# Kernel tuning notes

Measured on AMD Instinct MI355X. Metric: run time of the kernel, lower is better.

The kernel has to match this reference:

```python
import jax, jax.numpy as jnp
import numpy as np
from jax import lax

EPS = 1e-6
DT_RANK = 24  # ceil(384/16), Mamba convention
D_STATE = 16


def _ln(x, g, b, eps=EPS):
    m = jnp.mean(x, axis=-1, keepdims=True)
    v = jnp.mean((x - m) ** 2, axis=-1, keepdims=True)
    return (x - m) * lax.rsqrt(v + eps) * g + b


def setup_inputs() -> dict:
    key = jax.random.key(0)
    ks = jax.random.split(key, 10)
    B, Dd, Hh, Ww, C = 2, 8, 16, 16, 384
    di, ds, r = 384, D_STATE, DT_RANK  # d_inner = expand * d_model = 384
    s = 0.02
    f = lambda k, shape: (jax.random.normal(k, shape, jnp.float32) * s)
    return {
        "x": jax.random.normal(ks[0], (B, Dd, Hh, Ww, C), jnp.float32),
        "g1": jnp.ones((C,), jnp.float32), "b1": jnp.zeros((C,), jnp.float32),
        "W_in": f(ks[1], (C, 2 * di)), "b_in": jnp.zeros((2 * di,), jnp.float32),
        "conv_w": f(ks[2], (di, 1, 3, 3, 3)), "conv_b": jnp.zeros((di,), jnp.float32),
        "W_x": f(ks[3], (di, r + 2 * ds)),
        "W_dt": f(ks[4], (r, di)), "b_dt": jnp.zeros((di,), jnp.float32),
        "A_log": jnp.tile(jnp.log(jnp.arange(1, ds + 1, dtype=jnp.float32)), (di, 1)),
        "D_skip": jnp.ones((di,), jnp.float32),
        "on_g": jnp.ones((di,), jnp.float32), "on_b": jnp.zeros((di,), jnp.float32),
        "W_out": f(ks[5], (di, C)), "b_out": jnp.zeros((C,), jnp.float32),
        "g2": jnp.ones((C,), jnp.float32), "b2": jnp.zeros((C,), jnp.float32),
        "W1": f(ks[6], (C, C)), "b1m": jnp.zeros((C,), jnp.float32),
        "W2": f(ks[7], (C, C)), "b2m": jnp.zeros((C,), jnp.float32),
    }


def _ss3d(h, W_in, b_in, conv_w, conv_b, W_x, W_dt, b_dt, A_log, D_skip, on_g, on_b, W_out, b_out):
    # h: [B, D, H, W, C] -> Mamba-style selective scan over flattened DHW (orientation 0)
    B, Dd, Hh, Ww, C = h.shape
    di = W_in.shape[1] // 2
    ds = D_STATE
    L = Dd * Hh * Ww
    seq = h.reshape(B, L, C)
    xz = seq @ W_in + b_in                      # [B, L, 2*di]
    xin, z = jnp.split(xz, 2, axis=-1)
    # depthwise 3D conv + SiLU on the x branch
    xc = xin.reshape(B, Dd, Hh, Ww, di).transpose(0, 4, 1, 2, 3)  # [B, di, D, H, W]
    xc = lax.conv_general_dilated(xc, conv_w, (1, 1, 1), 'SAME',
                                  feature_group_count=di,
                                  dimension_numbers=('NCDHW', 'OIDHW', 'NCDHW'))
    xc = xc + conv_b[None, :, None, None, None]
    xin = jax.nn.silu(xc).transpose(0, 2, 3, 4, 1).reshape(B, L, di)
    # input-dependent dt, B, C
    dbc = xin @ W_x                              # [B, L, r + 2*ds]
    dt, Bm, Cm = jnp.split(dbc, [DT_RANK, DT_RANK + ds], axis=-1)
    dt = jax.nn.softplus(dt @ W_dt + b_dt)       # [B, L, di]
    A = -jnp.exp(A_log)                          # [di, ds]
    dA = jnp.exp(dt[..., None] * A)              # [B, L, di, ds]
    dBx = dt[..., None] * Bm[:, :, None, :] * xin[..., None]  # [B, L, di, ds]

    def step(carry, inp):
        da, dbx, c = inp                         # [B,di,ds], [B,di,ds], [B,ds]
        carry = da * carry + dbx
        y = jnp.einsum('bds,bs->bd', carry, c)
        return carry, y

    xs = (dA.transpose(1, 0, 2, 3), dBx.transpose(1, 0, 2, 3), Cm.transpose(1, 0, 2))
    h0 = jnp.zeros((B, di, ds), dA.dtype)
    _, ys = lax.scan(step, h0, xs)               # ys: [L, B, di]
    y = ys.transpose(1, 0, 2) + xin * D_skip
    y = _ln(y, on_g, on_b) * jax.nn.silu(z)
    out = y @ W_out + b_out
    return out.reshape(B, Dd, Hh, Ww, C)


def reference(x, g1, b1, W_in, b_in, conv_w, conv_b, W_x, W_dt, b_dt, A_log, D_skip,
              on_g, on_b, W_out, b_out, g2, b2, W1, b1m, W2, b2m):
    # x + SS3D(LN(x)); then x + MLP(LN(x)).  drop_path/dropout = 0 (eval)
    a = _ss3d(_ln(x, g1, b1), W_in, b_in, conv_w, conv_b, W_x, W_dt, b_dt,
              A_log, D_skip, on_g, on_b, W_out, b_out)
    x1 = x + a
    h2 = _ln(x1, g2, b2)
    mlp = jax.nn.gelu(h2 @ W1 + b1m) @ W2 + b2m
    return x1 + mlp
```

## Files before the change

kernel.cpp:

```cpp
#include <hip/hip_runtime.h>
#include <hip/hip_bf16.h>

using bf16 = __hip_bfloat16;
#define DEV __device__ __forceinline__

typedef __attribute__((ext_vector_type(8))) short short8;
typedef __attribute__((ext_vector_type(8))) unsigned short ushort8;
typedef __attribute__((ext_vector_type(4))) float f32x4;

constexpr int Bb = 2, DD = 8, HH = 16, WW = 16;
constexpr int C = 384, DI = 384, DS = 16, RR = 24;
constexpr int L = DD * HH * WW;
constexpr int M = Bb * L;

DEV bf16 f2b(float v) { return __float2bfloat16(v); }
DEV unsigned short f2bu(float v) {
    bf16 t = __float2bfloat16(v);
    unsigned short u; __builtin_memcpy(&u, &t, 2); return u;
}
DEV float braw(unsigned short u) {
    unsigned int x = ((unsigned int)u) << 16;
    float f; __builtin_memcpy(&f, &x, 4); return f;
}
DEV bool isbf(const unsigned short* g1p) { return g1p[0] == 0x3F80; }

typedef const __attribute__((address_space(1))) unsigned int* gaddr_t;
typedef __attribute__((address_space(3))) unsigned int* laddr_t;
DEV void gload_lds16(const void* g, void* l) {
    __builtin_amdgcn_global_load_lds((gaddr_t)g, (laddr_t)l, 16, 0, 0);
}

DEV float wred64(float v) {
    #pragma unroll
    for (int off = 32; off > 0; off >>= 1) v += __shfl_xor(v, off, 64);
    return v;
}
DEV float siluf(float x) { return x / (1.0f + __expf(-x)); }
DEV float softplusf(float x) { return (x > 15.0f) ? x : log1pf(__expf(x)); }
DEV float gelu_tanh(float x) {
    const float k0 = 0.7978845608028654f;
    float u = k0 * (x + 0.044715f * x * x * x);
    float e = __expf(2.0f * u);
    float t = 1.0f - 2.0f / (e + 1.0f);
    return 0.5f * x * (1.0f + t);
}

struct PrepTab {
    const void* tsrc[4];
    unsigned short* tdst[4];
    int tK[4], tN[4];
    const void* csrc[17];
    float* cdst[17];
    int coff[18];
};
__global__ __launch_bounds__(256) void prep_k(PrepTab t,
                                              const unsigned short* __restrict__ g1p,
                                              int ctotal) {
    bool fl = isbf(g1p);
    int z = blockIdx.z;
    if (z < 4) {
        __shared__ unsigned short tt[32][33];
        int N = t.tN[z], K = t.tK[z];
        int n0 = blockIdx.x * 32, k0 = blockIdx.y * 32;
        if (n0 >= N || k0 >= K) return;
        const void* src = t.tsrc[z];
        unsigned short* dst = t.tdst[z];
        int tx = threadIdx.x & 31, ty = threadIdx.x >> 5;
        #pragma unroll
        for (int i = 0; i < 4; i++) {
            int k = k0 + ty + i * 8;
            unsigned short u;
            if (fl) u = ((const unsigned short*)src)[(size_t)k * N + n0 + tx];
            else    u = f2bu(((const float*)src)[(size_t)k * N + n0 + tx]);
            tt[ty + i * 8][tx] = u;
        }
        __syncthreads();
        #pragma unroll
        for (int i = 0; i < 4; i++) {
            int n = n0 + ty + i * 8;
            dst[(size_t)n * K + k0 + tx] = tt[tx][ty + i * 8];
        }
    } else {
        int i = (blockIdx.y * 24 + blockIdx.x) * 256 + threadIdx.x;
        if (i >= ctotal) return;
        int seg = 0;
        #pragma unroll
        for (int k = 1; k < 18; k++) seg += (i >= t.coff[k]) ? 1 : 0;
        int j = i - t.coff[seg];
        const void* s = t.csrc[seg];
        float v = fl ? braw(((const unsigned short*)s)[j]) : ((const float*)s)[j];
        t.cdst[seg][j] = v;
    }
}

template <bool RAWIN>
__global__ __launch_bounds__(256) void ln_k(const void* __restrict__ xr,
                                            const float* __restrict__ g,
                                            const float* __restrict__ b,
                                            bf16* __restrict__ out,
                                            const unsigned short* __restrict__ g1p) {
    bool fl = RAWIN ? isbf(g1p) : false;
    int wave = blockIdx.x * 4 + (threadIdx.x >> 6);
    int lane = threadIdx.x & 63;
    size_t base = (size_t)wave * C;
    float v[6];
    #pragma unroll
    for (int j = 0; j < 6; j++) {
        size_t idx = base + lane + 64 * j;
        if (RAWIN && fl) v[j] = braw(((const unsigned short*)xr)[idx]);
        else             v[j] = ((const float*)xr)[idx];
    }
    float s = 0.f;
    #pragma unroll
    for (int j = 0; j < 6; j++) s += v[j];
    s = wred64(s);
    float mean = s * (1.0f / C);
    float q = 0.f;
    #pragma unroll
    for (int j = 0; j < 6; j++) { float d = v[j] - mean; q += d * d; }
    q = wred64(q);
    float rstd = rsqrtf(q * (1.0f / C) + 1e-6f);
    #pragma unroll
    for (int j = 0; j < 6; j++) {
        int c = lane + 64 * j;
        out[base + c] = f2b((v[j] - mean) * rstd * g[c] + b[c]);
    }
}

enum { EPI_XZT = 0, EPI_OUT = 1, EPI_GELU = 2, EPI_FINAL = 3 };

template <int N, int TN, int EPI>
__global__ __launch_bounds__(256) void gemm_mfma(const bf16* __restrict__ A,
                                                 const unsigned short* __restrict__ Bt,
                                                 const float* __restrict__ bias,
                                                 float* __restrict__ o0,
                                                 float* __restrict__ o1,
                                                 const float* __restrict__ auxf,
                                                 const void* __restrict__ auxraw,
                                                 void* __restrict__ obf,
                                                 const unsigned short* __restrict__ g1p) {
    __shared__ unsigned short Asb[128 * 32];
    __shared__ unsigned short Bsb[TN * 32];
    constexpr int MT = (TN == 128) ? 4 : 2;
    int tid = threadIdx.x;
    int m0 = blockIdx.x * 128, n0 = blockIdx.y * TN;
    int wid = tid >> 6, lane = tid & 63;
    int wm = (TN == 128) ? (wid >> 1) * 64 : wid * 32;
    int wn = (TN == 128) ? (wid & 1) * 64 : 0;
    int quad = lane >> 4, l15 = lane & 15;
    f32x4 acc[MT][4] = {};
    int srow = tid >> 2, sseg = (tid & 3) * 8;
    const unsigned short* Au = (const unsigned short*)A;
    for (int k0 = 0; k0 < 384; k0 += 32) {
        __syncthreads();
        gload_lds16(Au + (size_t)(m0 + srow) * 384 + k0 + sseg,
                    &Asb[srow * 32 + sseg]);
        gload_lds16(Au + (size_t)(m0 + 64 + srow) * 384 + k0 + sseg,
                    &Asb[(64 + srow) * 32 + sseg]);
        gload_lds16(Bt + (size_t)(n0 + srow) * 384 + k0 + sseg,
                    &Bsb[srow * 32 + sseg]);
        if constexpr (TN == 128)
            gload_lds16(Bt + (size_t)(n0 + 64 + srow) * 384 + k0 + sseg,
                        &Bsb[(64 + srow) * 32 + sseg]);
        __syncthreads();
        short8 af[MT], bfr[4];
        #pragma unroll
        for (int mt = 0; mt < MT; mt++)
            af[mt] = *(const short8*)&Asb[(wm + mt * 16 + l15) * 32 + quad * 8];
        #pragma unroll
        for (int nt = 0; nt < 4; nt++)
            bfr[nt] = *(const short8*)&Bsb[(wn + nt * 16 + l15) * 32 + quad * 8];
        #pragma unroll
        for (int mt = 0; mt < MT; mt++)
            #pragma unroll
            for (int nt = 0; nt < 4; nt++)
                acc[mt][nt] = __builtin_amdgcn_mfma_f32_16x16x32_bf16(
                    af[mt], bfr[nt], acc[mt][nt], 0, 0, 0);
    }
    bool fl = (EPI == EPI_FINAL || EPI == EPI_OUT) ? isbf(g1p) : false;
    #pragma unroll
    for (int mt = 0; mt < MT; mt++) {
        #pragma unroll
        for (int nt = 0; nt < 4; nt++) {
            int n = n0 + wn + nt * 16 + l15;
            int mb = m0 + wm + mt * 16 + quad * 4;
            float bi = bias[n];
            if constexpr (EPI == EPI_XZT) {
                f32x4 v = acc[mt][nt];
                v[0] += bi; v[1] += bi; v[2] += bi; v[3] += bi;
                float* dst = (n < 384) ? (o0 + (size_t)n * M + mb)
                                       : (o1 + (size_t)(n - 384) * M + mb);
                *(f32x4*)dst = v;
            } else {
                #pragma unroll
                for (int r = 0; r < 4; r++) {
                    int m = mb + r;
                    float v = acc[mt][nt][r] + bi;
                    if constexpr (EPI == EPI_OUT) {
                        float av;
                        if (fl) av = braw(((const unsigned short*)auxraw)[(size_t)m * 384 + n]);
                        else    av = ((const float*)auxraw)[(size_t)m * 384 + n];
                        o0[(size_t)m * 384 + n] = v + av;
                    } else if constexpr (EPI == EPI_GELU) {
                        ((bf16*)obf)[(size_t)m * 384 + n] = f2b(gelu_tanh(v));
                    } else {
                        float rr = v + auxf[(size_t)m * 384 + n];
                        if (fl) ((bf16*)obf)[(size_t)m * 384 + n] = f2b(rr);
                        else    ((float*)obf)[(size_t)m * 384 + n] = rr;
                    }
                }
            }
        }
    }
}

__global__ __launch_bounds__(256) void convT_k(const float* __restrict__ xT,
                                               const float* __restrict__ cw,
                                               const float* __restrict__ cb,
                                               float* __restrict__ xinT) {
    int c = blockIdx.y;
    int m0 = (blockIdx.x * 256 + threadIdx.x) * 4;
    int l = m0 & (L - 1);
    int d = l >> 8, h = (l >> 4) & 15, w0 = l & 15;
    const float* xc = xT + (size_t)c * M;
    const float* wc = cw + c * 27;
    float bias = cb[c];
    float acc[4] = {bias, bias, bias, bias};
    #pragma unroll
    for (int kd = -1; kd <= 1; kd++) {
        int dd = d + kd; if ((unsigned)dd >= 8u) continue;
        #pragma unroll
        for (int kh = -1; kh <= 1; kh++) {
            int hh = h + kh; if ((unsigned)hh >= 16u) continue;
            int mm = m0 + kd * 256 + kh * 16;
            float vv[6];
            vv[0] = (w0 == 0) ? 0.f : xc[mm - 1];
            float4 v14 = *(const float4*)(xc + mm);
            vv[1] = v14.x; vv[2] = v14.y; vv[3] = v14.z; vv[4] = v14.w;
            vv[5] = (w0 == 12) ? 0.f : xc[mm + 4];
            const float* wk = wc + (kd + 1) * 9 + (kh + 1) * 3;
            float wa = wk[0], wb = wk[1], wcc = wk[2];
            #pragma unroll
            for (int j = 0; j < 4; j++)
                acc[j] = fmaf(vv[j], wa, fmaf(vv[j + 1], wb, fmaf(vv[j + 2], wcc, acc[j])));
        }
    }
    float4 o = make_float4(siluf(acc[0]), siluf(acc[1]), siluf(acc[2]), siluf(acc[3]));
    *(float4*)(xinT + (size_t)c * M + m0) = o;
}

__global__ __launch_bounds__(256) void dbc2_k(const float* __restrict__ xinT,
                                              const float* __restrict__ Wx,
                                              float* __restrict__ part) {
    __shared__ float As[16][64];
    __shared__ float Ws[16 * 56];
    int tid = threadIdx.x;
    int m0 = blockIdx.x * 64;
    int kc = blockIdx.y;
    int tm = tid & 63, grp = tid >> 6;
    int kk = tid >> 4, mc = (tid & 15) * 4;
    float acc[14] = {};
    for (int k0 = kc * 64; k0 < kc * 64 + 64; k0 += 16) {
        float4 av = *(const float4*)(xinT + (size_t)(k0 + kk) * M + m0 + mc);
        __syncthreads();
        *(float4*)&As[kk][mc] = av;
        for (int idx = tid; idx < 16 * 56; idx += 256)
            Ws[idx] = Wx[k0 * 56 + idx];
        __syncthreads();
        #pragma unroll
        for (int k = 0; k < 16; k++) {
            float a = As[k][tm];
            #pragma unroll
            for (int jj = 0; jj < 14; jj++)
                acc[jj] = fmaf(a, Ws[k * 56 + grp * 14 + jj], acc[jj]);
        }
    }
    int m = m0 + tm;
    #pragma unroll
    for (int jj = 0; jj < 14; jj++) {
        int col = grp * 14 + jj;
        part[((size_t)kc * 56 + col) * M + m] = acc[jj];
    }
}

__global__ __launch_bounds__(256) void dbcfin_k(const float* __restrict__ part,
                                                const float* __restrict__ Wdt,
                                                const float* __restrict__ bdt,
                                                float* __restrict__ dtT,
                                                unsigned short* __restrict__ Brow,
                                                unsigned short* __restrict__ Crow) {
    __shared__ float dtr[24][64];
    int tid = threadIdx.x;
    int m0 = blockIdx.x * 64;
    int ng = blockIdx.y;
    for (int i = tid; i < 24 * 64; i += 256) {
        int col = i >> 6, mm = i & 63;
        float s = 0.f;
        #pragma unroll
        for (int kc = 0; kc < 6; kc++)
            s += part[((size_t)kc * 56 + col) * M + m0 + mm];
        dtr[col][mm] = s;
    }
    if (ng == 0) {
        for (int i = tid; i < 32 * 64; i += 256) {
            int col = 24 + (i >> 6), mm = i & 63;
            float s = 0.f;
            #pragma unroll
            for (int kc = 0; kc < 6; kc++)
                s += part[((size_t)kc * 56 + col) * M + m0 + mm];
            int m = m0 + mm;
            if (col < 40) Brow[(size_t)m * 16 + col - 24] = f2bu(s);
            else          Crow[(size_t)m * 16 + col - 40] = f2bu(s);
        }
    }
    __syncthreads();
    int mm = tid & 63, nq = tid >> 6;
    #pragma unroll 4
    for (int nj = 0; nj < 16; nj++) {
        int n = ng * 64 + nq * 16 + nj;
        float acc = bdt[n];
        #pragma unroll
        for (int j = 0; j < 24; j++)
            acc = fmaf(dtr[j][mm], Wdt[j * 384 + n], acc);
        dtT[(size_t)n * M + m0 + mm] = softplusf(acc);
    }
}

__global__ __launch_bounds__(128) void scan4_k(const float* __restrict__ dtT,
                                               const float* __restrict__ xinT,
                                               const unsigned short* __restrict__ Brow,
                                               const unsigned short* __restrict__ Crow,
                                               const float* __restrict__ alog,
                                               const float* __restrict__ dsk,
                                               float* __restrict__ yT) {
    __shared__ float dt_s[2112], x_s[2112];
    __shared__ float ypart[2 * 2112];
    int bi = blockIdx.x;
    int b = bi / DI, d = bi % DI;
    int wave = threadIdx.x >> 6, lane = threadIdx.x & 63;
    int s0 = wave * 8;
    float Aneg[8];
    #pragma unroll
    for (int ss = 0; ss < 8; ss++) Aneg[ss] = -__expf(alog[d * DS + s0 + ss]);
    const float* dtp = dtT + (size_t)d * M + b * L;
    const float* xp  = xinT + (size_t)d * M + b * L;
    #pragma unroll
    for (int i = 0; i < 4; i++) {
        int t4 = (threadIdx.x + i * 128) * 4;
        float4 dv = *(const float4*)(dtp + t4);
        float4 xv = *(const float4*)(xp + t4);
        int base = t4 + (t4 >> 5);
        dt_s[base + 0] = dv.x; dt_s[base + 1] = dv.y;
        dt_s[base + 2] = dv.z; dt_s[base + 3] = dv.w;
        x_s[base + 0] = xv.x; x_s[base + 1] = xv.y;
        x_s[base + 2] = xv.z; x_s[base + 3] = xv.w;
    }
    __syncthreads();
    const unsigned short* Bp = Brow + ((size_t)b * L) * 16 + s0;
    const unsigned short* Cp = Crow + ((size_t)b * L) * 16 + s0;
    int tbase = lane * 32;
    int pbase = lane * 33;
    float Ap[8], Bg[8];
    #pragma unroll
    for (int ss = 0; ss < 8; ss++) { Ap[ss] = 1.f; Bg[ss] = 0.f; }
    #pragma unroll 4
    for (int j = 0; j < 32; j++) {
        float dtv = dt_s[pbase + j];
        float dxv = dtv * x_s[pbase + j];
        ushort8 bu = *(const ushort8*)(Bp + (size_t)(tbase + j) * 16);
        #pragma unroll
        for (int ss = 0; ss < 8; ss++) {
            float dA = __expf(dtv * Aneg[ss]);
            Bg[ss] = fmaf(dA, Bg[ss], dxv * braw(bu[ss]));
            Ap[ss] *= dA;
        }
    }
    float carry[8];
    #pragma unroll
    for (int ss = 0; ss < 8; ss++) {
        float a = Ap[ss], bb = Bg[ss];
        #pragma unroll
        for (int off = 1; off < 64; off <<= 1) {
            float ap = __shfl_up(a, off, 64);
            float bp = __shfl_up(bb, off, 64);
            if (lane >= off) { bb = fmaf(a, bp, bb); a *= ap; }
        }
        float c = __shfl_up(bb, 1, 64);
        carry[ss] = (lane == 0) ? 0.f : c;
    }
    float* ypw = ypart + wave * 2112;
    float h[8];
    #pragma unroll
    for (int ss = 0; ss < 8; ss++) h[ss] = carry[ss];
    #pragma unroll 4
    for (int j = 0; j < 32; j++) {
        float dtv = dt_s[pbase + j];
        float dxv = dtv * x_s[pbase + j];
        size_t toff = (size_t)(tbase + j) * 16;
        ushort8 bu = *(const ushort8*)(Bp + toff);
        ushort8 cu = *(const ushort8*)(Cp + toff);
        float acc = 0.f;
        #pragma unroll
        for (int ss = 0; ss < 8; ss++) {
            float dA = __expf(dtv * Aneg[ss]);
            h[ss] = fmaf(dA, h[ss], dxv * braw(bu[ss]));
            acc = fmaf(h[ss], braw(cu[ss]), acc);
        }
        ypw[pbase + j] = acc;
    }
    __syncthreads();
    float Dv = dsk[d];
    float* yp = yT + (size_t)d * M + b * L;
    #pragma unroll
    for (int i = 0; i < 16; i++) {
        int t = threadIdx.x + 128 * i;
        int ti = t + (t >> 5);
        yp[t] = fmaf(x_s[ti], Dv, ypart[ti] + ypart[2112 + ti]);
    }
}

__global__ __launch_bounds__(256) void lnmulT_k(const float* __restrict__ yT,
                                                const float* __restrict__ zT,
                                                const float* __restrict__ g,
                                                const float* __restrict__ b,
                                                unsigned short* __restrict__ yact) {
    __shared__ float rs1[8][32], rs2[8][32];
    __shared__ float meanb[32], rstdb[32];
    __shared__ unsigned short tile[32][392];
    int moff = threadIdx.x & 31;
    int dsub = threadIdx.x >> 5;
    int m0 = blockIdx.x * 32;
    size_t mg = m0 + moff;
    float s1 = 0.f, s2 = 0.f;
    #pragma unroll 8
    for (int j = 0; j < 48; j++) {
        int d = dsub + 8 * j;
        float v = yT[(size_t)d * M + mg];
        s1 += v; s2 += v * v;
    }
    rs1[dsub][moff] = s1;
    rs2[dsub][moff] = s2;
    __syncthreads();
    if (threadIdx.x < 32) {
        float a1 = 0.f, a2 = 0.f;
        #pragma unroll
        for (int ss = 0; ss < 8; ss++) { a1 += rs1[ss][threadIdx.x]; a2 += rs2[ss][threadIdx.x]; }
        float mean = a1 * (1.0f / DI);
        float var = a2 * (1.0f / DI) - mean * mean;
        meanb[threadIdx.x] = mean;
        rstdb[threadIdx.x] = rsqrtf(var + 1e-6f);
    }
    __syncthreads();
    float mean = meanb[moff], rstd = rstdb[moff];
    #pragma unroll 8
    for (int j = 0; j < 48; j++) {
        int d = dsub + 8 * j;
        float v = yT[(size_t)d * M + mg];
        float ln = (v - mean) * rstd * g[d] + b[d];
        float zv = zT[(size_t)d * M + mg];
        tile[moff][d] = f2bu(ln * siluf(zv));
    }
    __syncthreads();
    #pragma unroll
    for (int i = 0; i < 6; i++) {
        int chunk = threadIdx.x + 256 * i;
        int row = chunk / 48, cc = chunk % 48;
        *(uint4*)(yact + ((size_t)(m0 + row)) * 384 + cc * 8) =
            *(const uint4*)&tile[row][cc * 8];
    }
}

extern "C" void kernel_launch(void* const* d_in, const int* in_sizes, int n_in,
                              void* d_out, int out_size, void* d_ws, size_t ws_size,
                              hipStream_t stream) {
    float* ws = (float*)d_ws;
    constexpr size_t S = (size_t)M * 384;
    bf16*  hb   = (bf16*)ws;
    float* xT   = ws + S / 2;
    float* zT   = xT + S;
    float* xinT = zT + S;
    float* dtT  = xinT + S;
    float* x1   = dtT + S;
    unsigned short* Brow = (unsigned short*)(x1 + S);
    unsigned short* Crow = Brow + (size_t)M * 16;
    float* part = (float*)(Crow + (size_t)M * 16);
    float* smalls = part + (size_t)6 * 56 * M;

    float* g1f  = smalls;        float* b1f  = g1f + 384;
    float* binf = b1f + 384;     float* cwf  = binf + 768;
    float* cbf  = cwf + 10368;   float* wxf  = cbf + 384;
    float* wdtf = wxf + 21504;   float* bdtf = wdtf + 9216;
    float* alogf= bdtf + 384;    float* dskf = alogf + 6144;
    float* ongf = dskf + 384;    float* onbf = ongf + 384;
    float* boutf= onbf + 384;    float* g2f  = boutf + 384;
    float* b2f_ = g2f + 384;     float* b1mf = b2f_ + 384;
    float* b2mf = b1mf + 384;
    unsigned short* WinT  = (unsigned short*)(b2mf + 384);
    unsigned short* WoutT = WinT + 294912;
    unsigned short* W1T   = WoutT + 147456;
    unsigned short* W2T   = W1T + 147456;

    float* yT = xT;
    bf16* h2b = hb;
    unsigned short* yactb = (unsigned short*)dtT;
    unsigned short* m1b = (unsigned short*)zT;
    const unsigned short* g1p = (const unsigned short*)d_in[1];

    PrepTab tab;
    {
        tab.tsrc[0] = d_in[3];  tab.tdst[0] = WinT;  tab.tK[0] = 384; tab.tN[0] = 768;
        tab.tsrc[1] = d_in[14]; tab.tdst[1] = WoutT; tab.tK[1] = 384; tab.tN[1] = 384;
        tab.tsrc[2] = d_in[18]; tab.tdst[2] = W1T;   tab.tK[2] = 384; tab.tN[2] = 384;
        tab.tsrc[3] = d_in[20]; tab.tdst[3] = W2T;   tab.tK[3] = 384; tab.tN[3] = 384;
        int idxs[17] = {1, 2, 4, 5, 6, 7, 8, 9, 10, 11, 12, 13, 15, 16, 17, 19, 21};
        float* dsts[17] = {g1f, b1f, binf, cwf, cbf, wxf, wdtf, bdtf, alogf, dskf,
                           ongf, onbf, boutf, g2f, b2f_, b1mf, b2mf};
        int ns[17] = {384, 384, 768, 10368, 384, 21504, 9216, 384, 6144, 384,
                      384, 384, 384, 384, 384, 384, 384};
        int off = 0;
        for (int k = 0; k < 17; k++) {
            tab.csrc[k] = d_in[idxs[k]];
            tab.cdst[k] = dsts[k];
            tab.coff[k] = off;
            off += ns[k];
        }
        tab.coff[17] = off;
        prep_k<<<dim3(24, 12, 5), 256, 0, stream>>>(tab, g1p, off);
    }

    ln_k<true><<<M / 4, 256, 0, stream>>>(d_in[0], g1f, b1f, hb, g1p);
    gemm_mfma<768, 128, EPI_XZT><<<dim3(M / 128, 6), 256, 0, stream>>>(
        hb, WinT, binf, xT, zT, nullptr, nullptr, nullptr, g1p);
    convT_k<<<dim3(M / 1024, DI), 256, 0, stream>>>(xT, cwf, cbf, xinT);
    dbc2_k<<<dim3(M / 64, 6), 256, 0, stream>>>(xinT, wxf, part);
    dbcfin_k<<<dim3(M / 64, 6), 256, 0, stream>>>(part, wdtf, bdtf, dtT, Brow, Crow);
    scan4_k<<<Bb * DI, 128, 0, stream>>>(dtT, xinT, Brow, Crow, alogf, dskf, yT);
    lnmulT_k<<<M / 32, 256, 0, stream>>>(yT, zT, ongf, onbf, yactb);
    gemm_mfma<384, 64, EPI_OUT><<<dim3(M / 128, 6), 256, 0, stream>>>(
        (const bf16*)yactb, WoutT, boutf, x1, nullptr, nullptr, d_in[0], nullptr, g1p);
    ln_k<false><<<M / 4, 256, 0, stream>>>(x1, g2f, b2f_, h2b, g1p);
    gemm_mfma<384, 64, EPI_GELU><<<dim3(M / 128, 6), 256, 0, stream>>>(
        h2b, W1T, b1mf, nullptr, nullptr, nullptr, nullptr, m1b, g1p);
    gemm_mfma<384, 64, EPI_FINAL><<<dim3(M / 128, 6), 256, 0, stream>>>(
        (const bf16*)m1b, W2T, b2mf, nullptr, nullptr, x1, nullptr, d_out, g1p);
}
```

Before: 232.0 us.

## Fuse first LayerNorm into prep kernel and second LayerNorm into out-projection GEMM

The first LayerNorm now runs as extra blocks (z==5) of the weight-prep kernel. It reads g1/b1 straight from the raw inputs, so it no longer waits on the converted copies and saves one launch. The output-projection GEMM is replaced by a full-row kernel: each block owns 64 rows and all 384 columns. It adds the residual, writes x1, and computes the second LayerNorm in registers with shuffle reductions, removing the separate ln_k pass and the re-read of x1. In exchange the fused GEMM has only 64 blocks, with large accumulator register use and a big B tile in LDS per block. It also computes variance as E[x²]−mean², which is less numerically stable.

```diff
diff --git a/kernel.cpp b/kernel.cpp
--- a/kernel.cpp
+++ b/kernel.cpp
@@ -54,14 +54,19 @@
     int coff[18];
 };
 __global__ __launch_bounds__(256) void prep_k(PrepTab t,
+                                              const void* __restrict__ xraw,
+                                              const void* __restrict__ g1raw,
+                                              const void* __restrict__ b1raw,
+                                              bf16* __restrict__ hb,
                                               const unsigned short* __restrict__ g1p,
                                               int ctotal) {
     bool fl = isbf(g1p);
     int z = blockIdx.z;
     if (z < 4) {
+        if (blockIdx.x >= 288) return;
         __shared__ unsigned short tt[32][33];
         int N = t.tN[z], K = t.tK[z];
-        int n0 = blockIdx.x * 32, k0 = blockIdx.y * 32;
+        int n0 = (blockIdx.x % 24) * 32, k0 = (blockIdx.x / 24) * 32;
         if (n0 >= N || k0 >= K) return;
         const void* src = t.tsrc[z];
         unsigned short* dst = t.tdst[z];
@@ -80,8 +85,8 @@
             int n = n0 + ty + i * 8;
             dst[(size_t)n * K + k0 + tx] = tt[tx][ty + i * 8];
         }
-    } else {
-        int i = (blockIdx.y * 24 + blockIdx.x) * 256 + threadIdx.x;
+    } else if (z == 4) {
+        int i = blockIdx.x * 256 + threadIdx.x;
         if (i >= ctotal) return;
         int seg = 0;
         #pragma unroll
@@ -90,44 +95,41 @@
         const void* s = t.csrc[seg];
         float v = fl ? braw(((const unsigned short*)s)[j]) : ((const float*)s)[j];
         t.cdst[seg][j] = v;
-    }
-}
-
-template <bool RAWIN>
-__global__ __launch_bounds__(256) void ln_k(const void* __restrict__ xr,
-                                            const float* __restrict__ g,
-                                            const float* __restrict__ b,
-                                            bf16* __restrict__ out,
-                                            const unsigned short* __restrict__ g1p) {
-    bool fl = RAWIN ? isbf(g1p) : false;
-    int wave = blockIdx.x * 4 + (threadIdx.x >> 6);
-    int lane = threadIdx.x & 63;
-    size_t base = (size_t)wave * C;
-    float v[6];
-    #pragma unroll
-    for (int j = 0; j < 6; j++) {
-        size_t idx = base + lane + 64 * j;
-        if (RAWIN && fl) v[j] = braw(((const unsigned short*)xr)[idx]);
-        else             v[j] = ((const float*)xr)[idx];
-    }
-    float s = 0.f;
-    #pragma unroll
-    for (int j = 0; j < 6; j++) s += v[j];
-    s = wred64(s);
-    float mean = s * (1.0f / C);
-    float q = 0.f;
-    #pragma unroll
-    for (int j = 0; j < 6; j++) { float d = v[j] - mean; q += d * d; }
-    q = wred64(q);
-    float rstd = rsqrtf(q * (1.0f / C) + 1e-6f);
-    #pragma unroll
-    for (int j = 0; j < 6; j++) {
-        int c = lane + 64 * j;
-        out[base + c] = f2b((v[j] - mean) * rstd * g[c] + b[c]);
-    }
-}
-
-enum { EPI_XZT = 0, EPI_OUT = 1, EPI_GELU = 2, EPI_FINAL = 3 };
+    } else {
+        int wave = blockIdx.x * 4 + (threadIdx.x >> 6);
+        int lane = threadIdx.x & 63;
+        size_t base = (size_t)wave * C;
+        float v[6];
+        #pragma unroll
+        for (int j = 0; j < 6; j++) {
+            size_t idx = base + lane + 64 * j;
+            if (fl) v[j] = braw(((const unsigned short*)xraw)[idx]);
+            else    v[j] = ((const float*)xraw)[idx];
+        }
+        float s = 0.f;
+        #pragma unroll
+        for (int j = 0; j < 6; j++) s += v[j];
+        s = wred64(s);
+        float mean = s * (1.0f / C);
+        float q = 0.f;
+        #pragma unroll
+        for (int j = 0; j < 6; j++) { float d = v[j] - mean; q += d * d; }
+        q = wred64(q);
+        float rstd = rsqrtf(q * (1.0f / C) + 1e-6f);
+        #pragma unroll
+        for (int j = 0; j < 6; j++) {
+            int c = lane + 64 * j;
+            float gv, bv;
+            if (fl) { gv = braw(((const unsigned short*)g1raw)[c]);
+                      bv = braw(((const unsigned short*)b1raw)[c]); }
+            else    { gv = ((const float*)g1raw)[c];
+                      bv = ((const float*)b1raw)[c]; }
+            hb[base + c] = f2b((v[j] - mean) * rstd * gv + bv);
+        }
+    }
+}
+
+enum { EPI_XZT = 0, EPI_GELU = 2, EPI_FINAL = 3 };
 
 template <int N, int TN, int EPI>
 __global__ __launch_bounds__(256) void gemm_mfma(const bf16* __restrict__ A,
@@ -136,7 +138,6 @@
                                                  float* __restrict__ o0,
                                                  float* __restrict__ o1,
                                                  const float* __restrict__ auxf,
-                                                 const void* __restrict__ auxraw,
                                                  void* __restrict__ obf,
                                                  const unsigned short* __restrict__ g1p) {
     __shared__ unsigned short Asb[128 * 32];
@@ -177,7 +178,7 @@
                 acc[mt][nt] = __builtin_amdgcn_mfma_f32_16x16x32_bf16(
                     af[mt], bfr[nt], acc[mt][nt], 0, 0, 0);
     }
-    bool fl = (EPI == EPI_FINAL || EPI == EPI_OUT) ? isbf(g1p) : false;
+    bool fl = (EPI == EPI_FINAL) ? isbf(g1p) : false;
     #pragma unroll
     for (int mt = 0; mt < MT; mt++) {
         #pragma unroll
@@ -196,12 +197,7 @@
                 for (int r = 0; r < 4; r++) {
                     int m = mb + r;
                     float v = acc[mt][nt][r] + bi;
-                    if constexpr (EPI == EPI_OUT) {
-                        float av;
-                        if (fl) av = braw(((const unsigned short*)auxraw)[(size_t)m * 384 + n]);
-                        else    av = ((const float*)auxraw)[(size_t)m * 384 + n];
-                        o0[(size_t)m * 384 + n] = v + av;
-                    } else if constexpr (EPI == EPI_GELU) {
+                    if constexpr (EPI == EPI_GELU) {
                         ((bf16*)obf)[(size_t)m * 384 + n] = f2b(gelu_tanh(v));
                     } else {
                         float rr = v + auxf[(size_t)m * 384 + n];
@@ -210,6 +206,85 @@
                     }
                 }
             }
+        }
+    }
+}
+
+__global__ __launch_bounds__(256) void gemmout_ln_k(
+        const unsigned short* __restrict__ A,
+        const unsigned short* __restrict__ Bt,
+        const float* __restrict__ bias,
+        const void* __restrict__ resid,
+        const float* __restrict__ g,
+        const float* __restrict__ b,
+        float* __restrict__ x1,
+        bf16* __restrict__ h2,
+        const unsigned short* __restrict__ g1p) {
+    __shared__ unsigned short Asb[64 * 32];
+    __shared__ unsigned short Bsb[384 * 32];
+    int tid = threadIdx.x;
+    int m0 = blockIdx.x * 64;
+    int wid = tid >> 6, lane = tid & 63;
+    int quad = lane >> 4, l15 = lane & 15;
+    f32x4 acc[24] = {};
+    int srow = tid >> 2, sseg = (tid & 3) * 8;
+    for (int k0 = 0; k0 < 384; k0 += 32) {
+        __syncthreads();
+        gload_lds16(A + (size_t)(m0 + srow) * 384 + k0 + sseg, &Asb[srow * 32 + sseg]);
+        #pragma unroll
+        for (int c = 0; c < 6; c++)
+            gload_lds16(Bt + (size_t)(c * 64 + srow) * 384 + k0 + sseg,
+                        &Bsb[(c * 64 + srow) * 32 + sseg]);
+        __syncthreads();
+        short8 af = *(const short8*)&Asb[(wid * 16 + l15) * 32 + quad * 8];
+        #pragma unroll
+        for (int nt = 0; nt < 24; nt++) {
+            short8 bfr = *(const short8*)&Bsb[(nt * 16 + l15) * 32 + quad * 8];
+            acc[nt] = __builtin_amdgcn_mfma_f32_16x16x32_bf16(af, bfr, acc[nt], 0, 0, 0);
+        }
+    }
+    bool fl = isbf(g1p);
+    float s1[4] = {0.f, 0.f, 0.f, 0.f}, s2[4] = {0.f, 0.f, 0.f, 0.f};
+    #pragma unroll
+    for (int nt = 0; nt < 24; nt++) {
+        int n = nt * 16 + l15;
+        float bi = bias[n];
+        #pragma unroll
+        for (int r = 0; r < 4; r++) {
+            int m = m0 + wid * 16 + quad * 4 + r;
+            float av;
+            if (fl) av = braw(((const unsigned short*)resid)[(size_t)m * 384 + n]);
+            else    av = ((const float*)resid)[(size_t)m * 384 + n];
+            float v = acc[nt][r] + bi + av;
+            acc[nt][r] = v;
+            x1[(size_t)m * 384 + n] = v;
+            s1[r] += v;
+            s2[r] += v * v;
+        }
+    }
+    #pragma unroll
+    for (int off = 1; off < 16; off <<= 1) {
+        #pragma unroll
+        for (int r = 0; r < 4; r++) {
+            s1[r] += __shfl_xor(s1[r], off, 64);
+            s2[r] += __shfl_xor(s2[r], off, 64);
+        }
+    }
+    float mean[4], rstd[4];
+    #pragma unroll
+    for (int r = 0; r < 4; r++) {
+        mean[r] = s1[r] * (1.0f / 384.0f);
+        float var = s2[r] * (1.0f / 384.0f) - mean[r] * mean[r];
+        rstd[r] = rsqrtf(var + 1e-6f);
+    }
+    #pragma unroll
+    for (int nt = 0; nt < 24; nt++) {
+        int n = nt * 16 + l15;
+        float gv = g[n], bv = b[n];
+        #pragma unroll
+        for (int r = 0; r < 4; r++) {
+            int m = m0 + wid * 16 + quad * 4 + r;
+            h2[(size_t)m * 384 + n] = f2b((acc[nt][r] - mean[r]) * rstd[r] * gv + bv);
         }
     }
 }
@@ -525,22 +600,21 @@
             off += ns[k];
         }
         tab.coff[17] = off;
-        prep_k<<<dim3(24, 12, 5), 256, 0, stream>>>(tab, g1p, off);
-    }
-
-    ln_k<true><<<M / 4, 256, 0, stream>>>(d_in[0], g1f, b1f, hb, g1p);
+        prep_k<<<dim3(1024, 1, 6), 256, 0, stream>>>(
+            tab, d_in[0], d_in[1], d_in[2], hb, g1p, off);
+    }
+
     gemm_mfma<768, 128, EPI_XZT><<<dim3(M / 128, 6), 256, 0, stream>>>(
-        hb, WinT, binf, xT, zT, nullptr, nullptr, nullptr, g1p);
+        hb, WinT, binf, xT, zT, nullptr, nullptr, g1p);
     convT_k<<<dim3(M / 1024, DI), 256, 0, stream>>>(xT, cwf, cbf, xinT);
     dbc2_k<<<dim3(M / 64, 6), 256, 0, stream>>>(xinT, wxf, part);
     dbcfin_k<<<dim3(M / 64, 6), 256, 0, stream>>>(part, wdtf, bdtf, dtT, Brow, Crow);
     scan4_k<<<Bb * DI, 128, 0, stream>>>(dtT, xinT, Brow, Crow, alogf, dskf, yT);
     lnmulT_k<<<M / 32, 256, 0, stream>>>(yT, zT, ongf, onbf, yactb);
-    gemm_mfma<384, 64, EPI_OUT><<<dim3(M / 128, 6), 256, 0, stream>>>(
-        (const bf16*)yactb, WoutT, boutf, x1, nullptr, nullptr, d_in[0], nullptr, g1p);
-    ln_k<false><<<M / 4, 256, 0, stream>>>(x1, g2f, b2f_, h2b, g1p);
+    gemmout_ln_k<<<M / 64, 256, 0, stream>>>(
+        yactb, WoutT, boutf, d_in[0], g2f, b2f_, x1, h2b, g1p);
     gemm_mfma<384, 64, EPI_GELU><<<dim3(M / 128, 6), 256, 0, stream>>>(
-        h2b, W1T, b1mf, nullptr, nullptr, nullptr, nullptr, m1b, g1p);
+        h2b, W1T, b1mf, nullptr, nullptr, nullptr, m1b, g1p);
     gemm_mfma<384, 64, EPI_FINAL><<<dim3(M / 128, 6), 256, 0, stream>>>(
-        (const bf16*)m1b, W2T, b2mf, nullptr, nullptr, x1, nullptr, d_out, g1p);
-}
+        (const bf16*)m1b, W2T, b2mf, nullptr, nullptr, x1, d_out, g1p);
+}
```

After: 254.1 us. 1.1x slower.
